# Optimization experiments

Hardware: AMD Instinct MI355X
Metric: run time of the kernel (lower is better)

The kernel has to match this reference:

```python
import math
import jax, jax.numpy as jnp
import numpy as np

S = 4096          # total packed tokens (b*s with bsz=1)
NUM_HEADS = 16
HEAD_DIM = 80
SCALE = 1.0 / math.sqrt(HEAD_DIM)


def setup_inputs() -> dict:
    key = jax.random.key(0)
    kq, kk, kv = jax.random.split(key, 3)
    q = jax.random.normal(kq, (S, NUM_HEADS, HEAD_DIM), dtype=jnp.float32)
    k = jax.random.normal(kk, (S, NUM_HEADS, HEAD_DIM), dtype=jnp.float32)
    v = jax.random.normal(kv, (S, NUM_HEADS, HEAD_DIM), dtype=jnp.float32)
    # 4 packed sequences of 1024 tokens each (flatten_batch=True, bsz=1)
    cu_seqlens = jnp.array([0, 1024, 2048, 3072, 4096], dtype=jnp.int32)
    return {"q": q, "k": k, "v": v, "bsz": 1, "cu_seqlens": cu_seqlens}


def reference(q, k, v, bsz, cu_seqlens):
    # q/k/v: [(b s), h, d]; flatten_batch=True so bsz == 1
    s = q.shape[0] // bsz
    h, d = q.shape[1], q.shape[2]

    # Block-diagonal mask from cu_seqlens: True inside each packed sequence.
    seg = jnp.searchsorted(cu_seqlens[1:], jnp.arange(s), side="right")  # [s]
    mask = seg[:, None] == seg[None, :]                                  # [s, s]

    # '(b s) h d -> b h s d'
    qb = q.reshape(bsz, s, h, d).transpose(0, 2, 1, 3)
    kb = k.reshape(bsz, s, h, d).transpose(0, 2, 1, 3)
    vb = v.reshape(bsz, s, h, d).transpose(0, 2, 1, 3)

    scores = jnp.einsum("bhsd,bhtd->bhst", qb, kb) * SCALE
    bias = jnp.where(mask, jnp.zeros((), scores.dtype), jnp.finfo(scores.dtype).min)
    attn = jax.nn.softmax((scores + bias).astype(jnp.float32), axis=-1).astype(q.dtype)

    out = jnp.einsum("bhst,bhtd->bhsd", attn, vb)
    # 'b h s d -> (b s) h d'
    return out.transpose(0, 2, 1, 3).reshape(bsz * s, h, d)
```

## Files before the change

### kernel.cpp

```cpp
#include <hip/hip_runtime.h>
#include <hip/hip_bf16.h>
#include <math.h>

#define NTOK 4096
#define NH 16
#define HD 80
#define TOKSTRIDE (NH * HD)
#define QBLK 64
#define KVBLK 64
#define KSTR 80
#define VSTR 72
#define PSTR 72

typedef __bf16 bf16x4 __attribute__((ext_vector_type(4)));
typedef __bf16 bf16x8 __attribute__((ext_vector_type(8)));
typedef float  f32x4  __attribute__((ext_vector_type(4)));
typedef short  short4v __attribute__((ext_vector_type(4)));

#if __has_builtin(__builtin_amdgcn_mfma_f32_16x16x16bf16_1k)
__device__ inline f32x4 mfma16(bf16x4 a, bf16x4 b, f32x4 c) {
  return __builtin_amdgcn_mfma_f32_16x16x16bf16_1k(
      __builtin_bit_cast(short4v, a), __builtin_bit_cast(short4v, b), c, 0, 0, 0);
}
#elif __has_builtin(__builtin_amdgcn_mfma_f32_16x16x16_bf16)
__device__ inline f32x4 mfma16(bf16x4 a, bf16x4 b, f32x4 c) {
  return __builtin_amdgcn_mfma_f32_16x16x16_bf16(a, b, c, 0, 0, 0);
}
#else
__device__ inline f32x4 mfma16(bf16x4 a, bf16x4 b, f32x4 c) {
  asm volatile("v_mfma_f32_16x16x16_bf16 %0, %1, %2, %0"
               : "+v"(c) : "v"(a), "v"(b));
  return c;
}
#endif

__global__ __launch_bounds__(256)
void prepack(const float* __restrict__ qg, const float* __restrict__ kg,
             const float* __restrict__ vg, __bf16* __restrict__ qb,
             __bf16* __restrict__ kb, __bf16* __restrict__ vtb) {
  __shared__ __align__(16) __bf16 Vl[HD][VSTR];
  const int tid  = threadIdx.x;
  const int tok0 = blockIdx.x * 64;
  const int h    = blockIdx.y;
  const float qscale = 1.4426950408889634f / sqrtf((float)HD);

  for (int i = tid; i < 64 * 20; i += 256) {
    const int row = i / 20;
    const int c4  = (i % 20) * 4;
    const size_t gsrc = (size_t)(tok0 + row) * TOKSTRIDE + h * HD + c4;
    const size_t gdst = ((size_t)h * NTOK + tok0 + row) * HD + c4;

    float4 fq = *reinterpret_cast<const float4*>(qg + gsrc);
    bf16x4 uq;
    uq[0] = (__bf16)(fq.x * qscale); uq[1] = (__bf16)(fq.y * qscale);
    uq[2] = (__bf16)(fq.z * qscale); uq[3] = (__bf16)(fq.w * qscale);
    *reinterpret_cast<bf16x4*>(qb + gdst) = uq;

    float4 fk = *reinterpret_cast<const float4*>(kg + gsrc);
    bf16x4 uk;
    uk[0] = (__bf16)fk.x; uk[1] = (__bf16)fk.y;
    uk[2] = (__bf16)fk.z; uk[3] = (__bf16)fk.w;
    *reinterpret_cast<bf16x4*>(kb + gdst) = uk;

    float4 fv = *reinterpret_cast<const float4*>(vg + gsrc);
    Vl[c4 + 0][row] = (__bf16)fv.x; Vl[c4 + 1][row] = (__bf16)fv.y;
    Vl[c4 + 2][row] = (__bf16)fv.z; Vl[c4 + 3][row] = (__bf16)fv.w;
  }
  __syncthreads();
  for (int i = tid; i < HD * 8; i += 256) {
    const int d  = i / 8;
    const int c8 = (i % 8) * 8;
    bf16x8 val = *reinterpret_cast<const bf16x8*>(&Vl[d][c8]);
    *reinterpret_cast<bf16x8*>(vtb + ((size_t)h * HD + d) * NTOK + tok0 + c8) = val;
  }
}

__global__ __launch_bounds__(256, 4)
void vis_attn11(const __bf16* __restrict__ qb, const __bf16* __restrict__ kb,
                const __bf16* __restrict__ vtb, const int* __restrict__ cu,
                int n_cu, float* __restrict__ outg) {
  __shared__ __align__(16) unsigned char smem[21920];
  __bf16* Kl = reinterpret_cast<__bf16*>(smem);
  __bf16* Vt = reinterpret_cast<__bf16*>(smem + 10400);

  const int tid  = threadIdx.x;
  const int w    = tid >> 6;
  const int lane = tid & 63;
  const int lr   = lane & 15;
  const int g    = lane >> 4;

  const int q0 = blockIdx.x * QBLK;
  const int h  = blockIdx.y;

  int kv_start = 0, kv_end = NTOK;
  for (int i = 0; i + 1 < n_cu; ++i) {
    int a = cu[i], b = cu[i + 1];
    if (q0 >= a && q0 < b) { kv_start = a; kv_end = b; }
  }

  if (tid < 16) Kl[KVBLK * KSTR + tid] = (__bf16)0.0f;

  const int qrow = q0 + w * 16 + lr;
  const __bf16* qrptr = qb + ((size_t)h * NTOK + qrow) * HD;
  bf16x8 qf[3];
  #pragma unroll
  for (int c = 0; c < 3; ++c) {
    const int dbase = c * 32 + g * 8;
    if (dbase < HD) {
      qf[c] = *reinterpret_cast<const bf16x8*>(qrptr + dbase);
    } else {
      #pragma unroll
      for (int j = 0; j < 8; ++j) qf[c][j] = (__bf16)0.0f;
    }
  }

  bf16x4 vfl;
  #pragma unroll
  for (int j = 0; j < 4; ++j) vfl[j] = (lr == 0) ? (__bf16)1.0f : (__bf16)0.0f;

  f32x4 O[6];
  #pragma unroll
  for (int n = 0; n < 6; ++n) O[n] = (f32x4){0.f, 0.f, 0.f, 0.f};

  const __bf16* kbh  = kb  + (size_t)h * NTOK * HD;
  const __bf16* vtbh = vtb + (size_t)h * HD * NTOK;
  const char* gbase = reinterpret_cast<const char*>(kbh);
  const int vdelta = (int)(reinterpret_cast<const char*>(vtbh) - gbase);

  int goff[5], ginc[5], ldsoff[5];
  #pragma unroll
  for (int j = 0; j < 5; ++j) {
    const int c = tid + j * 256;
    if (c < 640) {
      const int row = c / 10, col = (c % 10) * 8;
      goff[j]   = (kv_start * HD + row * HD + col) * 2;
      ginc[j]   = KVBLK * HD * 2;
      ldsoff[j] = (row * KSTR + col) * 2;
    } else {
      const int c2 = c - 640, d = c2 / 8, kc = (c2 % 8) * 8;
      goff[j]   = vdelta + (kv_start + d * NTOK + kc) * 2;
      ginc[j]   = KVBLK * 2;
      ldsoff[j] = 10400 + (d * VSTR + kc) * 2;
    }
  }

  bf16x8 st[5];
  #pragma unroll
  for (int j = 0; j < 5; ++j) {
    st[j] = *reinterpret_cast<const bf16x8*>(gbase + goff[j]);
    goff[j] += ginc[j];
  }

  for (int kv0 = kv_start; kv0 < kv_end; kv0 += KVBLK) {
    __syncthreads();
    #pragma unroll
    for (int j = 0; j < 5; ++j)
      *reinterpret_cast<bf16x8*>(smem + ldsoff[j]) = st[j];
    __syncthreads();

    if (kv0 + KVBLK < kv_end) {
      #pragma unroll
      for (int j = 0; j < 5; ++j) {
        st[j] = *reinterpret_cast<const bf16x8*>(gbase + goff[j]);
        goff[j] += ginc[j];
      }
    }

    bf16x4 pf[4];
    __builtin_amdgcn_s_setprio(1);
    #pragma unroll
    for (int t = 0; t < 4; ++t) {
      f32x4 S = (f32x4){0.f, 0.f, 0.f, 0.f};
      #pragma unroll
      for (int c = 0; c < 3; ++c) {
        bf16x8 kf = *reinterpret_cast<const bf16x8*>(&Kl[(t * 16 + lr) * KSTR + c * 32 + g * 8]);
        S = __builtin_amdgcn_mfma_f32_16x16x32_bf16(kf, qf[c], S, 0, 0, 0);
      }
      #pragma unroll
      for (int r = 0; r < 4; ++r)
        pf[t][r] = (__bf16)exp2f(S[r]);
    }
    __builtin_amdgcn_s_setprio(0);

    __builtin_amdgcn_s_setprio(1);
    #pragma unroll
    for (int n = 0; n < 5; ++n) {
      #pragma unroll
      for (int t = 0; t < 4; ++t) {
        bf16x4 vf = *reinterpret_cast<const bf16x4*>(&Vt[(n * 16 + lr) * VSTR + t * 16 + g * 4]);
        O[n] = mfma16(pf[t], vf, O[n]);
      }
    }
    #pragma unroll
    for (int t = 0; t < 4; ++t)
      O[5] = mfma16(pf[t], vfl, O[5]);
    __builtin_amdgcn_s_setprio(0);
  }

  float inv[4];
  #pragma unroll
  for (int r = 0; r < 4; ++r) {
    float l = __shfl(O[5][r], lane & 48);
    inv[r] = 1.0f / l;
  }
  const int orow0 = q0 + w * 16 + g * 4;
  #pragma unroll
  for (int n = 0; n < 5; ++n) {
    #pragma unroll
    for (int r = 0; r < 4; ++r)
      outg[(size_t)(orow0 + r) * TOKSTRIDE + h * HD + n * 16 + lr] = O[n][r] * inv[r];
  }
}

__global__ __launch_bounds__(256, 4)
void vis_attn_fb(const float* __restrict__ qg, const float* __restrict__ kg,
                 const float* __restrict__ vg, const int* __restrict__ cu,
                 int n_cu, float* __restrict__ outg) {
  __shared__ __align__(16) __bf16 Kl[KVBLK][104];
  __shared__ __align__(16) __bf16 Vt[HD][72];
  __shared__ __align__(16) __bf16 Pl[64][72];

  const int tid  = threadIdx.x;
  const int w    = tid >> 6;
  const int lane = tid & 63;
  const int lr   = lane & 15;
  const int g    = lane >> 4;
  const int q0 = blockIdx.x * 64;
  const int h  = blockIdx.y;

  int kv_start = 0, kv_end = NTOK;
  for (int i = 0; i + 1 < n_cu; ++i) {
    int a = cu[i], b = cu[i + 1];
    if (q0 >= a && q0 < b) { kv_start = a; kv_end = b; }
  }
  for (int i = tid; i < KVBLK * 16; i += 256)
    Kl[i >> 4][HD + (i & 15)] = (__bf16)0.0f;

  const float qscale = 1.4426950408889634f / sqrtf((float)HD);
  const int qrow = q0 + w * 16 + lr;
  const float* qptr = qg + (size_t)qrow * TOKSTRIDE + h * HD;
  bf16x8 qf[3];
  #pragma unroll
  for (int c = 0; c < 3; ++c) {
    const int dbase = c * 32 + g * 8;
    if (dbase < HD) {
      float4 f0 = *reinterpret_cast<const float4*>(qptr + dbase);
      float4 f1 = *reinterpret_cast<const float4*>(qptr + dbase + 4);
      qf[c][0] = (__bf16)(f0.x * qscale); qf[c][1] = (__bf16)(f0.y * qscale);
      qf[c][2] = (__bf16)(f0.z * qscale); qf[c][3] = (__bf16)(f0.w * qscale);
      qf[c][4] = (__bf16)(f1.x * qscale); qf[c][5] = (__bf16)(f1.y * qscale);
      qf[c][6] = (__bf16)(f1.z * qscale); qf[c][7] = (__bf16)(f1.w * qscale);
    } else {
      #pragma unroll
      for (int j = 0; j < 8; ++j) qf[c][j] = (__bf16)0.0f;
    }
  }

  f32x4 O[5];
  #pragma unroll
  for (int n = 0; n < 5; ++n) O[n] = (f32x4){0.f, 0.f, 0.f, 0.f};
  float m_run[4] = {-1e30f, -1e30f, -1e30f, -1e30f};
  float l_run[4] = {0.f, 0.f, 0.f, 0.f};

  for (int kv0 = kv_start; kv0 < kv_end; kv0 += KVBLK) {
    __syncthreads();
    for (int i = tid; i < KVBLK * (HD / 4); i += 256) {
      const int row = i / (HD / 4);
      const int c4  = (i % (HD / 4)) * 4;
      float4 f = *reinterpret_cast<const float4*>(
          kg + (size_t)(kv0 + row) * TOKSTRIDE + h * HD + c4);
      Kl[row][c4 + 0] = (__bf16)f.x; Kl[row][c4 + 1] = (__bf16)f.y;
      Kl[row][c4 + 2] = (__bf16)f.z; Kl[row][c4 + 3] = (__bf16)f.w;
    }
    for (int i = tid; i < KVBLK * (HD / 4); i += 256) {
      const int row = i / (HD / 4);
      const int c4  = (i % (HD / 4)) * 4;
      float4 f = *reinterpret_cast<const float4*>(
          vg + (size_t)(kv0 + row) * TOKSTRIDE + h * HD + c4);
      Vt[c4 + 0][row] = (__bf16)f.x; Vt[c4 + 1][row] = (__bf16)f.y;
      Vt[c4 + 2][row] = (__bf16)f.z; Vt[c4 + 3][row] = (__bf16)f.w;
    }
    __syncthreads();

    f32x4 S[4];
    #pragma unroll
    for (int t = 0; t < 4; ++t) {
      S[t] = (f32x4){0.f, 0.f, 0.f, 0.f};
      #pragma unroll
      for (int c = 0; c < 3; ++c) {
        bf16x8 kf = *reinterpret_cast<const bf16x8*>(&Kl[t * 16 + lr][c * 32 + g * 8]);
        S[t] = __builtin_amdgcn_mfma_f32_16x16x32_bf16(qf[c], kf, S[t], 0, 0, 0);
      }
    }
    float pmax[4];
    #pragma unroll
    for (int r = 0; r < 4; ++r)
      pmax[r] = fmaxf(fmaxf(S[0][r], S[1][r]), fmaxf(S[2][r], S[3][r]));
    #pragma unroll
    for (int r = 0; r < 4; ++r) {
      pmax[r] = fmaxf(pmax[r], __shfl_xor(pmax[r], 1));
      pmax[r] = fmaxf(pmax[r], __shfl_xor(pmax[r], 2));
      pmax[r] = fmaxf(pmax[r], __shfl_xor(pmax[r], 4));
      pmax[r] = fmaxf(pmax[r], __shfl_xor(pmax[r], 8));
    }
    float alpha[4];
    #pragma unroll
    for (int r = 0; r < 4; ++r) {
      float mn = fmaxf(m_run[r], pmax[r]);
      alpha[r] = exp2f(m_run[r] - mn);
      m_run[r] = mn;
    }
    #pragma unroll
    for (int t = 0; t < 4; ++t) {
      #pragma unroll
      for (int r = 0; r < 4; ++r)
        S[t][r] = exp2f(S[t][r] - m_run[r]);
    }
    float rsum[4];
    #pragma unroll
    for (int r = 0; r < 4; ++r) {
      rsum[r] = (S[0][r] + S[1][r]) + (S[2][r] + S[3][r]);
      rsum[r] += __shfl_xor(rsum[r], 1);
      rsum[r] += __shfl_xor(rsum[r], 2);
      rsum[r] += __shfl_xor(rsum[r], 4);
      rsum[r] += __shfl_xor(rsum[r], 8);
      l_run[r] = l_run[r] * alpha[r] + rsum[r];
    }
    #pragma unroll
    for (int n = 0; n < 5; ++n) {
      #pragma unroll
      for (int r = 0; r < 4; ++r) O[n][r] *= alpha[r];
    }
    #pragma unroll
    for (int t = 0; t < 4; ++t) {
      #pragma unroll
      for (int r = 0; r < 4; ++r)
        Pl[w * 16 + g * 4 + r][t * 16 + lr] = (__bf16)S[t][r];
    }
    #pragma unroll
    for (int kc = 0; kc < 2; ++kc) {
      bf16x8 pf = *reinterpret_cast<const bf16x8*>(&Pl[w * 16 + lr][kc * 32 + g * 8]);
      #pragma unroll
      for (int n = 0; n < 5; ++n) {
        bf16x8 vf = *reinterpret_cast<const bf16x8*>(&Vt[n * 16 + lr][kc * 32 + g * 8]);
        O[n] = __builtin_amdgcn_mfma_f32_16x16x32_bf16(pf, vf, O[n], 0, 0, 0);
      }
    }
  }

  float inv[4];
  #pragma unroll
  for (int r = 0; r < 4; ++r) inv[r] = 1.0f / l_run[r];
  const int orow0 = q0 + w * 16 + g * 4;
  #pragma unroll
  for (int n = 0; n < 5; ++n) {
    #pragma unroll
    for (int r = 0; r < 4; ++r)
      outg[(size_t)(orow0 + r) * TOKSTRIDE + h * HD + n * 16 + lr] = O[n][r] * inv[r];
  }
}

extern "C" void kernel_launch(void* const* d_in, const int* in_sizes, int n_in,
                              void* d_out, int out_size, void* d_ws, size_t ws_size,
                              hipStream_t stream) {
  const float* q  = (const float*)d_in[0];
  const float* k  = (const float*)d_in[1];
  const float* v  = (const float*)d_in[2];
  const int* cu   = (const int*)d_in[4];
  const int n_cu  = in_sizes[4];
  float* out      = (float*)d_out;

  const size_t one = (size_t)NH * NTOK * HD * sizeof(__bf16);

  if (ws_size >= 3 * one) {
    __bf16* qb  = (__bf16*)d_ws;
    __bf16* kb  = (__bf16*)((char*)d_ws + one);
    __bf16* vtb = (__bf16*)((char*)d_ws + 2 * one);
    dim3 gp(NTOK / 64, NH);
    prepack<<<gp, 256, 0, stream>>>(q, k, v, qb, kb, vtb);
    dim3 ga(NTOK / QBLK, NH);
    vis_attn11<<<ga, 256, 0, stream>>>(qb, kb, vtb, cu, n_cu, out);
  } else {
    dim3 gf(NTOK / 64, NH);
    vis_attn_fb<<<gf, 256, 0, stream>>>(q, k, v, cu, n_cu, out);
  }
}
```

Measured before the change: 63.33 us.

## Load Q directly in attention kernel and permute V layout for wide LDS reads

Drops the Q bf16 prepack pass so the attention kernel reads fp32 Q straight from global memory and scales and converts it in registers. This removes one workspace write and re-read. The V transpose in prepack now permutes 4-token groups so the attention kernel can fetch each lane's V fragments with two 16-byte LDS loads instead of four 8-byte ones. LDS strides for K and V change to reduce bank conflicts, and K row padding is zeroed. The cost is more global traffic per block for fp32 Q and extra shuffle work.

```diff
diff --git a/kernel.cpp b/kernel.cpp
--- a/kernel.cpp
+++ b/kernel.cpp
@@ -8,9 +8,9 @@
 #define TOKSTRIDE (NH * HD)
 #define QBLK 64
 #define KVBLK 64
-#define KSTR 80
-#define VSTR 72
-#define PSTR 72
+#define KSTR 88
+#define VSTR 68
+#define KLBYTES (65 * KSTR * 2)
 
 typedef __bf16 bf16x4 __attribute__((ext_vector_type(4)));
 typedef __bf16 bf16x8 __attribute__((ext_vector_type(8)));
@@ -35,14 +35,12 @@
 #endif
 
 __global__ __launch_bounds__(256)
-void prepack(const float* __restrict__ qg, const float* __restrict__ kg,
-             const float* __restrict__ vg, __bf16* __restrict__ qb,
+void prepack(const float* __restrict__ kg, const float* __restrict__ vg,
              __bf16* __restrict__ kb, __bf16* __restrict__ vtb) {
-  __shared__ __align__(16) __bf16 Vl[HD][VSTR];
+  __shared__ __align__(16) __bf16 Vl[HD][72];
   const int tid  = threadIdx.x;
   const int tok0 = blockIdx.x * 64;
   const int h    = blockIdx.y;
-  const float qscale = 1.4426950408889634f / sqrtf((float)HD);
 
   for (int i = tid; i < 64 * 20; i += 256) {
     const int row = i / 20;
@@ -50,12 +48,6 @@
     const size_t gsrc = (size_t)(tok0 + row) * TOKSTRIDE + h * HD + c4;
     const size_t gdst = ((size_t)h * NTOK + tok0 + row) * HD + c4;
 
-    float4 fq = *reinterpret_cast<const float4*>(qg + gsrc);
-    bf16x4 uq;
-    uq[0] = (__bf16)(fq.x * qscale); uq[1] = (__bf16)(fq.y * qscale);
-    uq[2] = (__bf16)(fq.z * qscale); uq[3] = (__bf16)(fq.w * qscale);
-    *reinterpret_cast<bf16x4*>(qb + gdst) = uq;
-
     float4 fk = *reinterpret_cast<const float4*>(kg + gsrc);
     bf16x4 uk;
     uk[0] = (__bf16)fk.x; uk[1] = (__bf16)fk.y;
@@ -67,21 +59,22 @@
     Vl[c4 + 2][row] = (__bf16)fv.z; Vl[c4 + 3][row] = (__bf16)fv.w;
   }
   __syncthreads();
-  for (int i = tid; i < HD * 8; i += 256) {
-    const int d  = i / 8;
-    const int c8 = (i % 8) * 8;
-    bf16x8 val = *reinterpret_cast<const bf16x8*>(&Vl[d][c8]);
-    *reinterpret_cast<bf16x8*>(vtb + ((size_t)h * HD + d) * NTOK + tok0 + c8) = val;
+  for (int i = tid; i < HD * 16; i += 256) {
+    const int d = i / 16;
+    const int b = i % 16;
+    const int pb = ((b & 3) << 2) | (b >> 2);
+    bf16x4 val = *reinterpret_cast<const bf16x4*>(&Vl[d][b * 4]);
+    *reinterpret_cast<bf16x4*>(vtb + ((size_t)h * HD + d) * NTOK + tok0 + pb * 4) = val;
   }
 }
 
 __global__ __launch_bounds__(256, 4)
-void vis_attn11(const __bf16* __restrict__ qb, const __bf16* __restrict__ kb,
+void vis_attn12(const float* __restrict__ qg, const __bf16* __restrict__ kb,
                 const __bf16* __restrict__ vtb, const int* __restrict__ cu,
                 int n_cu, float* __restrict__ outg) {
-  __shared__ __align__(16) unsigned char smem[21920];
+  __shared__ __align__(16) unsigned char smem[22320];
   __bf16* Kl = reinterpret_cast<__bf16*>(smem);
-  __bf16* Vt = reinterpret_cast<__bf16*>(smem + 10400);
+  __bf16* Vt = reinterpret_cast<__bf16*>(smem + KLBYTES);
 
   const int tid  = threadIdx.x;
   const int w    = tid >> 6;
@@ -98,16 +91,25 @@
     if (q0 >= a && q0 < b) { kv_start = a; kv_end = b; }
   }
 
-  if (tid < 16) Kl[KVBLK * KSTR + tid] = (__bf16)0.0f;
-
+  for (int i = tid; i < 512 + KSTR; i += 256) {
+    if (i < 512) Kl[(i >> 3) * KSTR + 80 + (i & 7)] = (__bf16)0.0f;
+    else         Kl[64 * KSTR + (i - 512)]          = (__bf16)0.0f;
+  }
+
+  const float qscale = 1.4426950408889634f / sqrtf((float)HD);
   const int qrow = q0 + w * 16 + lr;
-  const __bf16* qrptr = qb + ((size_t)h * NTOK + qrow) * HD;
+  const float* qrp = qg + (size_t)qrow * TOKSTRIDE + h * HD;
   bf16x8 qf[3];
   #pragma unroll
   for (int c = 0; c < 3; ++c) {
     const int dbase = c * 32 + g * 8;
     if (dbase < HD) {
-      qf[c] = *reinterpret_cast<const bf16x8*>(qrptr + dbase);
+      float4 f0 = *reinterpret_cast<const float4*>(qrp + dbase);
+      float4 f1 = *reinterpret_cast<const float4*>(qrp + dbase + 4);
+      qf[c][0] = (__bf16)(f0.x * qscale); qf[c][1] = (__bf16)(f0.y * qscale);
+      qf[c][2] = (__bf16)(f0.z * qscale); qf[c][3] = (__bf16)(f0.w * qscale);
+      qf[c][4] = (__bf16)(f1.x * qscale); qf[c][5] = (__bf16)(f1.y * qscale);
+      qf[c][6] = (__bf16)(f1.z * qscale); qf[c][7] = (__bf16)(f1.w * qscale);
     } else {
       #pragma unroll
       for (int j = 0; j < 8; ++j) qf[c][j] = (__bf16)0.0f;
@@ -140,7 +142,7 @@
       const int c2 = c - 640, d = c2 / 8, kc = (c2 % 8) * 8;
       goff[j]   = vdelta + (kv_start + d * NTOK + kc) * 2;
       ginc[j]   = KVBLK * 2;
-      ldsoff[j] = 10400 + (d * VSTR + kc) * 2;
+      ldsoff[j] = KLBYTES + (d * VSTR + kc) * 2;
     }
   }
 
@@ -185,11 +187,16 @@
     __builtin_amdgcn_s_setprio(1);
     #pragma unroll
     for (int n = 0; n < 5; ++n) {
-      #pragma unroll
-      for (int t = 0; t < 4; ++t) {
-        bf16x4 vf = *reinterpret_cast<const bf16x4*>(&Vt[(n * 16 + lr) * VSTR + t * 16 + g * 4]);
-        O[n] = mfma16(pf[t], vf, O[n]);
-      }
+      bf16x8 v01 = *reinterpret_cast<const bf16x8*>(&Vt[(n * 16 + lr) * VSTR + g * 16]);
+      bf16x8 v23 = *reinterpret_cast<const bf16x8*>(&Vt[(n * 16 + lr) * VSTR + g * 16 + 8]);
+      bf16x4 vf0 = __builtin_shufflevector(v01, v01, 0, 1, 2, 3);
+      bf16x4 vf1 = __builtin_shufflevector(v01, v01, 4, 5, 6, 7);
+      bf16x4 vf2 = __builtin_shufflevector(v23, v23, 0, 1, 2, 3);
+      bf16x4 vf3 = __builtin_shufflevector(v23, v23, 4, 5, 6, 7);
+      O[n] = mfma16(pf[0], vf0, O[n]);
+      O[n] = mfma16(pf[1], vf1, O[n]);
+      O[n] = mfma16(pf[2], vf2, O[n]);
+      O[n] = mfma16(pf[3], vf3, O[n]);
     }
     #pragma unroll
     for (int t = 0; t < 4; ++t)
@@ -372,14 +379,13 @@
 
   const size_t one = (size_t)NH * NTOK * HD * sizeof(__bf16);
 
-  if (ws_size >= 3 * one) {
-    __bf16* qb  = (__bf16*)d_ws;
-    __bf16* kb  = (__bf16*)((char*)d_ws + one);
-    __bf16* vtb = (__bf16*)((char*)d_ws + 2 * one);
+  if (ws_size >= 2 * one) {
+    __bf16* kbuf = (__bf16*)d_ws;
+    __bf16* vtb  = (__bf16*)((char*)d_ws + one);
     dim3 gp(NTOK / 64, NH);
-    prepack<<<gp, 256, 0, stream>>>(q, k, v, qb, kb, vtb);
+    prepack<<<gp, 256, 0, stream>>>(k, v, kbuf, vtb);
     dim3 ga(NTOK / QBLK, NH);
-    vis_attn11<<<ga, 256, 0, stream>>>(qb, kb, vtb, cu, n_cu, out);
+    vis_attn12<<<ga, 256, 0, stream>>>(q, kbuf, vtb, cu, n_cu, out);
   } else {
     dim3 gf(NTOK / 64, NH);
     vis_attn_fb<<<gf, 256, 0, stream>>>(q, k, v, cu, n_cu, out);
```

After: 111.4 us. 1.76x slower.
